# Optimization experiments

Measured on AMD Instinct MI355X. Metric: run time of the kernel, lower is better.

Reference implementation:

```python
import jax, jax.numpy as jnp
import numpy as np

TOP_K = 2

def setup_inputs() -> dict:
    key = jax.random.key(0)
    k1, k2, k3, k4 = jax.random.split(key, 4)
    B, S, D, E = 4, 2048, 2048, 8
    x = jax.random.normal(k1, (B, S, D), dtype=jnp.float32)
    router_w = jax.random.normal(k2, (D, E), dtype=jnp.float32) * 0.02
    expert_w = jax.random.normal(k3, (E, D, D), dtype=jnp.float32) * 0.02
    expert_b = jax.random.normal(k4, (E, D), dtype=jnp.float32) * 0.02
    return {"x": x, "router_w": router_w, "expert_w": expert_w, "expert_b": expert_b}

def reference(x, router_w, expert_w, expert_b):
    # Router + top-k dispatch (computed as in the original, but its results are
    # DISCARDED by the original forward -- the masked expert loop does `pass`).
    router_logits = jnp.einsum('bsd,de->bse', x, router_w)
    routing_weights = jax.nn.softmax(router_logits, axis=-1)
    weights, selected_experts = jax.lax.top_k(routing_weights, TOP_K)
    weights = weights / jnp.sum(weights, axis=-1, keepdims=True)  # dead code
    _ = (weights, selected_experts)
    # The original returns self.experts[0](x): expert 0 applied to ALL tokens.
    out = jnp.einsum('bsd,od->bso', x, expert_w[0]) + expert_b[0]
    return out
```

## Files before the change

### kernel.cpp

```cpp
#include <hip/hip_runtime.h>
#include <hip/hip_bf16.h>
#include <stdint.h>


#define M_DIM 8192
#define N_DIM 2048
#define K_DIM 2048
#define BM 128
#define BN 128
#define BK 32

typedef __attribute__((ext_vector_type(8))) short bf16x8;
typedef __attribute__((ext_vector_type(4))) float f32x4;

__device__ __forceinline__ unsigned short f2bf(float f) {
    union { float f; uint32_t u; } v; v.f = f;
    uint32_t u = v.u;
    uint32_t r = (u + 0x7fffu + ((u >> 16) & 1u)) >> 16;
    return (unsigned short)r;
}

__global__ __launch_bounds__(256) void cvt_f32_to_bf16(
        const float* __restrict__ x, const float* __restrict__ w,
        unsigned short* __restrict__ xb, unsigned short* __restrict__ wb,
        int nx4, int nw4) {
    const int stride = gridDim.x * blockDim.x;
    const int i0 = blockIdx.x * blockDim.x + threadIdx.x;
    for (int i = i0; i < nx4; i += stride) {
        float4 v = ((const float4*)x)[i];
        ushort4 o;
        o.x = f2bf(v.x); o.y = f2bf(v.y); o.z = f2bf(v.z); o.w = f2bf(v.w);
        ((ushort4*)xb)[i] = o;
    }
    for (int i = i0; i < nw4; i += stride) {
        float4 v = ((const float4*)w)[i];
        ushort4 o;
        o.x = f2bf(v.x); o.y = f2bf(v.y); o.z = f2bf(v.z); o.w = f2bf(v.w);
        ((ushort4*)wb)[i] = o;
    }
}

__global__ __launch_bounds__(256) void gemm_bt_bias(
        const unsigned short* __restrict__ A,
        const unsigned short* __restrict__ B,
        const float* __restrict__ bias,
        float* __restrict__ C) {
    __shared__ unsigned short As[BM * BK];
    __shared__ unsigned short Bs[BN * BK];

    const int t    = threadIdx.x;
    const int lane = t & 63;
    const int wv   = t >> 6;
    const int wm   = wv >> 1;
    const int wn   = wv & 1;

    const int bid = blockIdx.x;
    const int bm  = bid >> 4;
    const int bn  = bid & 15;

    const int row16 = lane & 15;
    const int kb    = (lane >> 4) << 3;

    const int srow = lane >> 2;
    const int scol = (lane & 3) << 3;

    f32x4 acc[4][4];
#pragma unroll
    for (int i = 0; i < 4; ++i)
#pragma unroll
        for (int j = 0; j < 4; ++j)
            acc[i][j] = (f32x4){0.f, 0.f, 0.f, 0.f};

    const size_t a_base = (size_t)(bm * BM) * K_DIM;
    const size_t b_base = (size_t)(bn * BN) * K_DIM;

    for (int k0 = 0; k0 < K_DIM; k0 += BK) {
#pragma unroll
        for (int r = 0; r < 2; ++r) {
            const int chunk = wv * 2 + r;
            const unsigned short* ga =
                A + a_base + (size_t)(chunk * 16 + srow) * K_DIM + k0 + scol;
            __builtin_amdgcn_global_load_lds(
                (const __attribute__((address_space(1))) void*)ga,
                (__attribute__((address_space(3))) void*)&As[chunk * 16 * BK],
                16, 0, 0);
            const unsigned short* gb =
                B + b_base + (size_t)(chunk * 16 + srow) * K_DIM + k0 + scol;
            __builtin_amdgcn_global_load_lds(
                (const __attribute__((address_space(1))) void*)gb,
                (__attribute__((address_space(3))) void*)&Bs[chunk * 16 * BK],
                16, 0, 0);
        }
        __syncthreads();

        bf16x8 af[4], bq[4];
#pragma unroll
        for (int mi = 0; mi < 4; ++mi)
            af[mi] = *(const bf16x8*)&As[(wm * 64 + mi * 16 + row16) * BK + kb];
#pragma unroll
        for (int ni = 0; ni < 4; ++ni)
            bq[ni] = *(const bf16x8*)&Bs[(wn * 64 + ni * 16 + row16) * BK + kb];

#pragma unroll
        for (int mi = 0; mi < 4; ++mi)
#pragma unroll
            for (int ni = 0; ni < 4; ++ni)
                acc[mi][ni] = __builtin_amdgcn_mfma_f32_16x16x32_bf16(
                    af[mi], bq[ni], acc[mi][ni], 0, 0, 0);

        __syncthreads();
    }

    float bv[4];
#pragma unroll
    for (int ni = 0; ni < 4; ++ni)
        bv[ni] = bias[bn * BN + wn * 64 + ni * 16 + row16];

    const int rrow = (lane >> 4) * 4;
#pragma unroll
    for (int mi = 0; mi < 4; ++mi) {
#pragma unroll
        for (int ni = 0; ni < 4; ++ni) {
            const int col = bn * BN + wn * 64 + ni * 16 + row16;
#pragma unroll
            for (int j = 0; j < 4; ++j) {
                const int row = bm * BM + wm * 64 + mi * 16 + rrow + j;
                C[(size_t)row * N_DIM + col] = acc[mi][ni][j] + bv[ni];
            }
        }
    }
}

extern "C" void kernel_launch(void* const* d_in, const int* in_sizes, int n_in,
                              void* d_out, int out_size, void* d_ws, size_t ws_size,
                              hipStream_t stream) {
    const float* x        = (const float*)d_in[0];
    const float* expert_w = (const float*)d_in[2];
    const float* expert_b = (const float*)d_in[3];
    float* out = (float*)d_out;

    unsigned short* xb = (unsigned short*)d_ws;
    unsigned short* wb = xb + (size_t)M_DIM * K_DIM;

    const int nx4 = (M_DIM * K_DIM) / 4;
    const int nw4 = (N_DIM * K_DIM) / 4;

    cvt_f32_to_bf16<<<2048, 256, 0, stream>>>(x, expert_w, xb, wb, nx4, nw4);

    dim3 grid((M_DIM / BM) * (N_DIM / BN));
    gemm_bt_bias<<<grid, 256, 0, stream>>>(xb, wb, expert_b, out);
}
```

Before: 312.7 us.

## Rewrite GEMM with 256x256 tiles, triple-buffered LDS pipeline and swizzled layout

Replaces the 128x128 single-buffered GEMM with a 512-thread, 256x256-tile kernel. It prefetches two K-steps ahead into three LDS buffers using direct global-to-LDS loads and needs one barrier per step instead of two. It also XOR-swizzles the LDS layout to avoid bank conflicts, raises wave priority around the MFMA bursts, remaps blocks for L2 locality, and widens the conversion kernel to 8 elements per thread. The cost is higher register and LDS use, allowing one block per CU, and a grid of only 256 blocks, which may leave some CUs underused.

New measurement: 287.2 us. -8.2%, faster.

```diff
diff --git a/kernel.cpp b/kernel.cpp
--- a/kernel.cpp
+++ b/kernel.cpp
@@ -6,12 +6,16 @@
 #define M_DIM 8192
 #define N_DIM 2048
 #define K_DIM 2048
-#define BM 128
-#define BN 128
+#define BM 256
+#define BN 256
 #define BK 32
+#define NT (K_DIM / BK)
+#define BUF_ELEMS 16384
+#define LDS_BYTES (3 * BUF_ELEMS * 2)
 
 typedef __attribute__((ext_vector_type(8))) short bf16x8;
 typedef __attribute__((ext_vector_type(4))) float f32x4;
+typedef __attribute__((ext_vector_type(8))) unsigned short u16x8;
 
 __device__ __forceinline__ unsigned short f2bf(float f) {
     union { float f; uint32_t u; } v; v.f = f;
@@ -22,109 +26,155 @@
 
 __global__ __launch_bounds__(256) void cvt_f32_to_bf16(
         const float* __restrict__ x, const float* __restrict__ w,
-        unsigned short* __restrict__ xb, unsigned short* __restrict__ wb,
-        int nx4, int nw4) {
+        unsigned short* __restrict__ xb, unsigned short* __restrict__ wb) {
+    const int NX8 = (M_DIM * K_DIM) / 8;
+    const int NW8 = (N_DIM * K_DIM) / 8;
     const int stride = gridDim.x * blockDim.x;
-    const int i0 = blockIdx.x * blockDim.x + threadIdx.x;
-    for (int i = i0; i < nx4; i += stride) {
-        float4 v = ((const float4*)x)[i];
-        ushort4 o;
-        o.x = f2bf(v.x); o.y = f2bf(v.y); o.z = f2bf(v.z); o.w = f2bf(v.w);
-        ((ushort4*)xb)[i] = o;
-    }
-    for (int i = i0; i < nw4; i += stride) {
-        float4 v = ((const float4*)w)[i];
-        ushort4 o;
-        o.x = f2bf(v.x); o.y = f2bf(v.y); o.z = f2bf(v.z); o.w = f2bf(v.w);
-        ((ushort4*)wb)[i] = o;
-    }
-}
-
-__global__ __launch_bounds__(256) void gemm_bt_bias(
+    for (int i = blockIdx.x * blockDim.x + threadIdx.x; i < NX8 + NW8; i += stride) {
+        const float4* s; unsigned short* d; int j;
+        if (i < NX8) { s = (const float4*)x; d = xb; j = i; }
+        else         { s = (const float4*)w; d = wb; j = i - NX8; }
+        float4 a = s[2 * j];
+        float4 b = s[2 * j + 1];
+        u16x8 o;
+        o[0] = f2bf(a.x); o[1] = f2bf(a.y); o[2] = f2bf(a.z); o[3] = f2bf(a.w);
+        o[4] = f2bf(b.x); o[5] = f2bf(b.y); o[6] = f2bf(b.z); o[7] = f2bf(b.w);
+        *(u16x8*)(d + (size_t)8 * j) = o;
+    }
+}
+
+__device__ __forceinline__ int swzE(int row, int colByte) {
+    int b = (row << 6) | colByte;
+    b ^= ((b >> 7) & 3) << 4;
+    return b >> 1;
+}
+
+__device__ __forceinline__ void stage_half(const unsigned short* g,
+                                           unsigned short* ldsDst) {
+    __builtin_amdgcn_global_load_lds(
+        (const __attribute__((address_space(1))) void*)g,
+        (__attribute__((address_space(3))) void*)ldsDst, 16, 0, 0);
+}
+
+__global__ __launch_bounds__(512, 1) void gemm_bt_pipe(
         const unsigned short* __restrict__ A,
         const unsigned short* __restrict__ B,
         const float* __restrict__ bias,
         float* __restrict__ C) {
-    __shared__ unsigned short As[BM * BK];
-    __shared__ unsigned short Bs[BN * BK];
-
-    const int t    = threadIdx.x;
-    const int lane = t & 63;
-    const int wv   = t >> 6;
-    const int wm   = wv >> 1;
-    const int wn   = wv & 1;
+    extern __shared__ unsigned short lds[];
+
+    const int tid  = threadIdx.x;
+    const int lane = tid & 63;
+    const int wv   = tid >> 6;
+    const int wm   = wv >> 2;
+    const int wn   = wv & 3;
 
     const int bid = blockIdx.x;
-    const int bm  = bid >> 4;
-    const int bn  = bid & 15;
-
-    const int row16 = lane & 15;
-    const int kb    = (lane >> 4) << 3;
-
-    const int srow = lane >> 2;
-    const int scol = (lane & 3) << 3;
-
-    f32x4 acc[4][4];
-#pragma unroll
-    for (int i = 0; i < 4; ++i)
+    const int lb  = (bid & 7) * 32 + (bid >> 3);
+    const int bm0 = (lb & 31) * BM;
+    const int bn0 = (lb >> 5) * BN;
+
+    const unsigned short* Ag = A + (size_t)bm0 * K_DIM;
+    const unsigned short* Bg = B + (size_t)bn0 * K_DIM;
+
+    const int lin0 = wv * 1024 + lane * 16;
+    const int lin1 = 8192 + lin0;
+    const int s0 = lin0 ^ (((lin0 >> 7) & 3) << 4);
+    const int s1 = lin1 ^ (((lin1 >> 7) & 3) << 4);
+    const size_t gofs0 = (size_t)(s0 >> 6) * K_DIM + ((s0 & 63) >> 1);
+    const size_t gofs1 = (size_t)(s1 >> 6) * K_DIM + ((s1 & 63) >> 1);
+    const int dst0 = (wv * 1024) >> 1;
+    const int dst1 = (8192 + wv * 1024) >> 1;
+
+    const int r16  = lane & 15;
+    const int c16b = (lane >> 4) << 4;
+    int offA[8], offB[4];
+#pragma unroll
+    for (int mi = 0; mi < 8; ++mi)
+        offA[mi] = swzE(wm * 128 + mi * 16 + r16, c16b);
+#pragma unroll
+    for (int ni = 0; ni < 4; ++ni)
+        offB[ni] = 8192 + swzE(wn * 64 + ni * 16 + r16, c16b);
+
+    f32x4 acc[8][4];
+#pragma unroll
+    for (int i = 0; i < 8; ++i)
 #pragma unroll
         for (int j = 0; j < 4; ++j)
             acc[i][j] = (f32x4){0.f, 0.f, 0.f, 0.f};
 
-    const size_t a_base = (size_t)(bm * BM) * K_DIM;
-    const size_t b_base = (size_t)(bn * BN) * K_DIM;
-
-    for (int k0 = 0; k0 < K_DIM; k0 += BK) {
-#pragma unroll
-        for (int r = 0; r < 2; ++r) {
-            const int chunk = wv * 2 + r;
-            const unsigned short* ga =
-                A + a_base + (size_t)(chunk * 16 + srow) * K_DIM + k0 + scol;
-            __builtin_amdgcn_global_load_lds(
-                (const __attribute__((address_space(1))) void*)ga,
-                (__attribute__((address_space(3))) void*)&As[chunk * 16 * BK],
-                16, 0, 0);
-            const unsigned short* gb =
-                B + b_base + (size_t)(chunk * 16 + srow) * K_DIM + k0 + scol;
-            __builtin_amdgcn_global_load_lds(
-                (const __attribute__((address_space(1))) void*)gb,
-                (__attribute__((address_space(3))) void*)&Bs[chunk * 16 * BK],
-                16, 0, 0);
+#pragma unroll
+    for (int tt = 0; tt < 2; ++tt) {
+        unsigned short* sA = lds + tt * BUF_ELEMS;
+        unsigned short* sB = sA + 8192;
+        const int k0 = tt * BK;
+        stage_half(Ag + gofs0 + k0, sA + dst0);
+        stage_half(Ag + gofs1 + k0, sA + dst1);
+        stage_half(Bg + gofs0 + k0, sB + dst0);
+        stage_half(Bg + gofs1 + k0, sB + dst1);
+    }
+    asm volatile("s_waitcnt vmcnt(4)" ::: "memory");
+    __builtin_amdgcn_s_barrier();
+    asm volatile("" ::: "memory");
+
+    int cb = 0, sb = 2;
+    for (int t = 0; t < NT; ++t) {
+        unsigned short* cbuf = lds + cb * BUF_ELEMS;
+        unsigned short* sA   = lds + sb * BUF_ELEMS;
+        unsigned short* sB   = sA + 8192;
+        const int k2 = (t + 2) * BK;
+        const bool doS = (t + 2) < NT;
+
+        bf16x8 bfr[4];
+#pragma unroll
+        for (int ni = 0; ni < 4; ++ni)
+            bfr[ni] = *(const bf16x8*)(cbuf + offB[ni]);
+
+#pragma unroll
+        for (int ph = 0; ph < 4; ++ph) {
+            if (doS) {
+                if      (ph == 0) stage_half(Ag + gofs0 + k2, sA + dst0);
+                else if (ph == 1) stage_half(Ag + gofs1 + k2, sA + dst1);
+                else if (ph == 2) stage_half(Bg + gofs0 + k2, sB + dst0);
+                else              stage_half(Bg + gofs1 + k2, sB + dst1);
+            }
+            bf16x8 a0 = *(const bf16x8*)(cbuf + offA[2 * ph]);
+            bf16x8 a1 = *(const bf16x8*)(cbuf + offA[2 * ph + 1]);
+            __builtin_amdgcn_s_setprio(1);
+#pragma unroll
+            for (int ni = 0; ni < 4; ++ni)
+                acc[2 * ph][ni] = __builtin_amdgcn_mfma_f32_16x16x32_bf16(
+                    a0, bfr[ni], acc[2 * ph][ni], 0, 0, 0);
+#pragma unroll
+            for (int ni = 0; ni < 4; ++ni)
+                acc[2 * ph + 1][ni] = __builtin_amdgcn_mfma_f32_16x16x32_bf16(
+                    a1, bfr[ni], acc[2 * ph + 1][ni], 0, 0, 0);
+            __builtin_amdgcn_s_setprio(0);
         }
-        __syncthreads();
-
-        bf16x8 af[4], bq[4];
-#pragma unroll
-        for (int mi = 0; mi < 4; ++mi)
-            af[mi] = *(const bf16x8*)&As[(wm * 64 + mi * 16 + row16) * BK + kb];
-#pragma unroll
-        for (int ni = 0; ni < 4; ++ni)
-            bq[ni] = *(const bf16x8*)&Bs[(wn * 64 + ni * 16 + row16) * BK + kb];
-
-#pragma unroll
-        for (int mi = 0; mi < 4; ++mi)
-#pragma unroll
-            for (int ni = 0; ni < 4; ++ni)
-                acc[mi][ni] = __builtin_amdgcn_mfma_f32_16x16x32_bf16(
-                    af[mi], bq[ni], acc[mi][ni], 0, 0, 0);
-
-        __syncthreads();
+
+        if (doS) asm volatile("s_waitcnt vmcnt(4)" ::: "memory");
+        else     asm volatile("s_waitcnt vmcnt(0)" ::: "memory");
+        __builtin_amdgcn_s_barrier();
+        asm volatile("" ::: "memory");
+
+        cb = (cb == 2) ? 0 : cb + 1;
+        sb = (sb == 2) ? 0 : sb + 1;
     }
 
     float bv[4];
 #pragma unroll
     for (int ni = 0; ni < 4; ++ni)
-        bv[ni] = bias[bn * BN + wn * 64 + ni * 16 + row16];
+        bv[ni] = bias[bn0 + wn * 64 + ni * 16 + r16];
 
     const int rrow = (lane >> 4) * 4;
 #pragma unroll
-    for (int mi = 0; mi < 4; ++mi) {
+    for (int mi = 0; mi < 8; ++mi) {
 #pragma unroll
         for (int ni = 0; ni < 4; ++ni) {
-            const int col = bn * BN + wn * 64 + ni * 16 + row16;
+            const int col = bn0 + wn * 64 + ni * 16 + r16;
 #pragma unroll
             for (int j = 0; j < 4; ++j) {
-                const int row = bm * BM + wm * 64 + mi * 16 + rrow + j;
+                const int row = bm0 + wm * 128 + mi * 16 + rrow + j;
                 C[(size_t)row * N_DIM + col] = acc[mi][ni][j] + bv[ni];
             }
         }
@@ -142,11 +192,10 @@
     unsigned short* xb = (unsigned short*)d_ws;
     unsigned short* wb = xb + (size_t)M_DIM * K_DIM;
 
-    const int nx4 = (M_DIM * K_DIM) / 4;
-    const int nw4 = (N_DIM * K_DIM) / 4;
-
-    cvt_f32_to_bf16<<<2048, 256, 0, stream>>>(x, expert_w, xb, wb, nx4, nw4);
-
-    dim3 grid((M_DIM / BM) * (N_DIM / BN));
-    gemm_bt_bias<<<grid, 256, 0, stream>>>(xb, wb, expert_b, out);
-}
+    cvt_f32_to_bf16<<<2048, 256, 0, stream>>>(x, expert_w, xb, wb);
+
+    (void)hipFuncSetAttribute((const void*)gemm_bt_pipe,
+                              hipFuncAttributeMaxDynamicSharedMemorySize,
+                              LDS_BYTES);
+    gemm_bt_pipe<<<dim3(256), dim3(512), LDS_BYTES, stream>>>(xb, wb, expert_b, out);
+}
```
